# Performance work log

Hardware: AMD Instinct MI355X
Metric: run time of the kernel (lower is better)

## Reference

```python
import jax, jax.numpy as jnp
import numpy as np

EMBED_DIM = 2048
NUM_HEADS = 16
NUM_GROUPS = 4
HEAD_DIM = EMBED_DIM // NUM_HEADS  # 128
B, S = 2, 2048


def setup_inputs() -> dict:
    key = jax.random.key(0)
    ks = jax.random.split(key, 7)
    sc = 0.02
    return {
        "x": jax.random.normal(ks[0], (B, S, EMBED_DIM), dtype=jnp.float32),
        "Wq": jax.random.normal(ks[1], (EMBED_DIM, EMBED_DIM), dtype=jnp.float32) * sc,
        "bq": jnp.zeros((EMBED_DIM,), dtype=jnp.float32),
        "Wkv": jax.random.normal(ks[2], (EMBED_DIM, 2 * EMBED_DIM // NUM_GROUPS), dtype=jnp.float32) * sc,
        "bkv": jnp.zeros((2 * EMBED_DIM // NUM_GROUPS,), dtype=jnp.float32),
        "Wo": jax.random.normal(ks[3], (EMBED_DIM, EMBED_DIM), dtype=jnp.float32) * sc,
        "bo": jnp.zeros((EMBED_DIM,), dtype=jnp.float32),
    }


def reference(x, Wq, bq, Wkv, bkv, Wo, bo):
    b, s, e = x.shape
    group_size = NUM_HEADS // NUM_GROUPS
    # projections (torch Linear: x @ W + b with W stored [in, out] here)
    q = (x @ Wq + bq).reshape(b, s, NUM_HEADS, HEAD_DIM).transpose(0, 2, 1, 3)   # [B,H,S,D]
    kv = (x @ Wkv + bkv).reshape(b, s, NUM_GROUPS, 2 * HEAD_DIM).transpose(0, 2, 1, 3)  # [B,G,S,2D]
    k, v = kv[..., :HEAD_DIM], kv[..., HEAD_DIM:]                                # [B,G,S,D]
    # repeat each kv group for its heads (matches repeat_interleave on head dim)
    k = jnp.repeat(k, group_size, axis=1)                                        # [B,H,S,D]
    v = jnp.repeat(v, group_size, axis=1)                                        # [B,H,S,D]
    scores = jnp.einsum("bhqd,bhkd->bhqk", q, k) / (HEAD_DIM ** 0.5)             # [B,H,S,S]
    attn = jax.nn.softmax(scores, axis=-1)
    out = jnp.einsum("bhqk,bhkd->bhqd", attn, v)                                 # [B,H,S,D]
    out = out.transpose(0, 2, 1, 3).reshape(b, s, e)
    return out @ Wo + bo
```

## Files before the change

kernel.cpp:

```cpp
#include <hip/hip_runtime.h>

#define DEV __device__ __forceinline__

typedef unsigned short u16;
typedef unsigned int u32;
using bf16x8 = __attribute__((ext_vector_type(8))) __bf16;
using f32x4v = __attribute__((ext_vector_type(4))) float;

typedef __attribute__((address_space(1))) void gas_void;
typedef __attribute__((address_space(3))) void las_void;

DEV u16 f32_bf16(float f){
  u32 u = __float_as_uint(f);
  u += 0x7FFFu + ((u >> 16) & 1u);
  return (u16)(u >> 16);
}
DEV float bf16_f32(u16 h){ return __uint_as_float(((u32)h) << 16); }

DEV void gload16(const void* g, void* l){
  __builtin_amdgcn_global_load_lds((gas_void*)g, (las_void*)l, 16, 0, 0);
}

__global__ void cvt_f32_bf16_k(const float* __restrict__ in, u16* __restrict__ out, int n){
  int i = (blockIdx.x * 256 + threadIdx.x) * 8;
  if (i >= n) return;
  float4 a = *(const float4*)(in + i);
  float4 b = *(const float4*)(in + i + 4);
  uint4 r;
  r.x = (u32)f32_bf16(a.x) | ((u32)f32_bf16(a.y) << 16);
  r.y = (u32)f32_bf16(a.z) | ((u32)f32_bf16(a.w) << 16);
  r.z = (u32)f32_bf16(b.x) | ((u32)f32_bf16(b.y) << 16);
  r.w = (u32)f32_bf16(b.z) | ((u32)f32_bf16(b.w) << 16);
  *(uint4*)(out + i) = r;
}

template<typename T>
__global__ void transpose_cvt_k(const T* __restrict__ in, u16* __restrict__ out, int R, int C){
  in  += (size_t)blockIdx.z * R * C;
  out += (size_t)blockIdx.z * R * C;
  __shared__ float tile[64][65];
  int c0 = blockIdx.x * 64, r0 = blockIdx.y * 64;
  int t = threadIdx.x;
  int lr = t >> 4;
  int lc = (t & 15) * 4;
  #pragma unroll
  for (int p = 0; p < 4; p++){
    int row = p * 16 + lr;
    const T* src = in + (size_t)(r0 + row) * C + c0 + lc;
    float v0, v1, v2, v3;
    if constexpr (sizeof(T) == 4){
      float4 v = *(const float4*)src;
      v0 = v.x; v1 = v.y; v2 = v.z; v3 = v.w;
    } else {
      ushort4 v = *(const ushort4*)src;
      v0 = bf16_f32(v.x); v1 = bf16_f32(v.y); v2 = bf16_f32(v.z); v3 = bf16_f32(v.w);
    }
    tile[row][lc+0] = v0; tile[row][lc+1] = v1; tile[row][lc+2] = v2; tile[row][lc+3] = v3;
  }
  __syncthreads();
  #pragma unroll
  for (int p = 0; p < 4; p++){
    int ocol = p * 16 + lr;
    ushort4 w;
    w.x = f32_bf16(tile[lc+0][ocol]);
    w.y = f32_bf16(tile[lc+1][ocol]);
    w.z = f32_bf16(tile[lc+2][ocol]);
    w.w = f32_bf16(tile[lc+3][ocol]);
    *(ushort4*)(out + (size_t)(c0 + ocol) * R + r0 + lc) = w;
  }
}

__global__ __launch_bounds__(256, 2)
void gemm_bf16_k(const u16* __restrict__ A, const u16* __restrict__ BT,
                 const float* __restrict__ bias,
                 u16* __restrict__ outU0, u16* __restrict__ outU1,
                 float* __restrict__ outF,
                 int M, int N, int K, int mode)
{
  __shared__ __align__(16) u16 sA[2][128*32];
  __shared__ __align__(16) u16 sB[2][128*32];
  const int t = threadIdx.x;
  const int l = t & 63;
  const int wv = t >> 6;
  const int wm = wv >> 1, wn = wv & 1;
  const int rl = l & 15, gr = l >> 4;
  const size_t m0 = (size_t)blockIdx.x * 128, n0 = (size_t)blockIdx.y * 128;

  const u16* gA = A + m0 * K;
  const u16* gB = BT + n0 * K;

  f32x4v acc[4][4];
  #pragma unroll
  for (int i = 0; i < 4; i++)
    #pragma unroll
    for (int j = 0; j < 4; j++)
      acc[i][j] = (f32x4v)(0.0f);

  auto stage = [&](int buf, int kt){
    const size_t k0 = (size_t)kt * 32;
    #pragma unroll
    for (int i = 0; i < 2; i++){
      int c = i * 256 + t;
      int row = c >> 2, kc = c & 3;
      gload16(gA + (size_t)row * K + k0 + kc * 8, &sA[buf][c * 8]);
      gload16(gB + (size_t)row * K + k0 + kc * 8, &sB[buf][c * 8]);
    }
  };

  auto compute = [&](int buf){
    const u16* sa = sA[buf];
    const u16* sb = sB[buf];
    bf16x8 af[4], bfr[4];
    #pragma unroll
    for (int mr = 0; mr < 4; mr++)
      af[mr] = *(const bf16x8*)(sa + (wm*64 + mr*16 + rl)*32 + gr*8);
    #pragma unroll
    for (int nr = 0; nr < 4; nr++)
      bfr[nr] = *(const bf16x8*)(sb + (wn*64 + nr*16 + rl)*32 + gr*8);
    __builtin_amdgcn_s_setprio(1);
    #pragma unroll
    for (int mr = 0; mr < 4; mr++)
      #pragma unroll
      for (int nr = 0; nr < 4; nr++)
        acc[mr][nr] = __builtin_amdgcn_mfma_f32_16x16x32_bf16(af[mr], bfr[nr], acc[mr][nr], 0, 0, 0);
    __builtin_amdgcn_s_setprio(0);
  };

  stage(0, 0);
  asm volatile("s_waitcnt vmcnt(0)" ::: "memory");
  __syncthreads();
  const int NT = K / 32;
  for (int kt = 0; kt < NT; kt++){
    int cur = kt & 1;
    if (kt + 1 < NT) stage(cur ^ 1, kt + 1);
    compute(cur);
    asm volatile("s_waitcnt vmcnt(0)" ::: "memory");
    __syncthreads();
  }

  #pragma unroll
  for (int nr = 0; nr < 4; nr++){
    int col = (int)n0 + wn*64 + nr*16 + rl;
    float bv = bias[col];
    #pragma unroll
    for (int mr = 0; mr < 4; mr++){
      int rowb = (int)m0 + wm*64 + mr*16 + gr*4;
      #pragma unroll
      for (int r = 0; r < 4; r++){
        int row = rowb + r;
        float v = acc[mr][nr][r] + bv;
        if (mode == 2){
          outF[(size_t)row * N + col] = v;
        } else if (mode == 0){
          int b = row >> 11, s = row & 2047, h = col >> 7, d = col & 127;
          outU0[(((size_t)(b*16 + h)) * 2048 + s) * 128 + d] = f32_bf16(v);
        } else {
          int b = row >> 11, s = row & 2047, g = col >> 8, c = col & 255;
          u16* dst = (c < 128) ? outU0 : outU1;
          dst[(((size_t)(b*4 + g)) * 2048 + s) * 128 + (c & 127)] = f32_bf16(v);
        }
      }
    }
  }
}

__global__ __launch_bounds__(256, 2)
void attn_k(const u16* __restrict__ Q, const u16* __restrict__ Kb,
            const u16* __restrict__ VT, u16* __restrict__ O)
{
  __shared__ __align__(16) u16 sK[2][64*128];
  __shared__ __align__(16) u16 sV[2][128*64];
  __shared__ __align__(16) u16 Plds[4][16*72];
  const int t = threadIdx.x, l = t & 63, wv = t >> 6;
  const int rl = l & 15, gr = l >> 4;
  const int bh = blockIdx.y;
  const int b = bh >> 4, h = bh & 15, g = h >> 2;
  const int q0 = blockIdx.x * 64 + wv * 16;
  const u16* Qp = Q + ((size_t)(b*16 + h) * 2048 + q0) * 128;
  const u16* Kp = Kb + (size_t)(b*4 + g) * 2048 * 128;
  const u16* Vp = VT + (size_t)(b*4 + g) * 128 * 2048;

  bf16x8 qf[4];
  #pragma unroll
  for (int ds = 0; ds < 4; ds++)
    qf[ds] = *(const bf16x8*)(Qp + rl*128 + ds*32 + gr*8);

  f32x4v acc_o[8];
  #pragma unroll
  for (int i = 0; i < 8; i++) acc_o[i] = (f32x4v)(0.0f);
  float m_run = -3.0e38f, l_run = 0.0f;
  const float scale = 0.0883883476483184f;

  auto stageKV = [&](int buf, int kt){
    const int kv0 = kt * 64;
    const u16* Ksrc = Kp + (size_t)kv0 * 128;
    #pragma unroll
    for (int j = 0; j < 4; j++){
      int n16 = j * 256 + t;
      int row = n16 >> 4;
      int cl  = n16 & 15;
      int sc  = cl ^ (row & 7);
      gload16(Ksrc + row * 128 + sc * 8, &sK[buf][n16 * 8]);
    }
    const u16* Vsrc = Vp + kv0;
    #pragma unroll
    for (int j = 0; j < 4; j++){
      int n16 = j * 256 + t;
      int row = n16 >> 3;
      int cl  = n16 & 7;
      int sc  = cl ^ (row & 7);
      gload16(Vsrc + (size_t)row * 2048 + sc * 8, &sV[buf][n16 * 8]);
    }
  };

  stageKV(0, 0);
  asm volatile("s_waitcnt vmcnt(0)" ::: "memory");
  __syncthreads();

  for (int kt = 0; kt < 32; kt++){
    const int cur = kt & 1;
    if (kt + 1 < 32) stageKV(cur ^ 1, kt + 1);
    const u16* sk = sK[cur];
    const u16* sv = sV[cur];

    float pv[4][4];
    float tm = -3.0e38f;
    #pragma unroll
    for (int tt = 0; tt < 4; tt++){
      f32x4v st = (f32x4v)(0.0f);
      bf16x8 kf[4];
      #pragma unroll
      for (int ds = 0; ds < 4; ds++){
        int r = tt*16 + rl;
        int c = ds*4 + gr;
        kf[ds] = *(const bf16x8*)(sk + r*128 + ((c ^ (r & 7)) * 8));
      }
      __builtin_amdgcn_s_setprio(1);
      #pragma unroll
      for (int ds = 0; ds < 4; ds++)
        st = __builtin_amdgcn_mfma_f32_16x16x32_bf16(kf[ds], qf[ds], st, 0, 0, 0);
      __builtin_amdgcn_s_setprio(0);
      #pragma unroll
      for (int r = 0; r < 4; r++){
        float s = st[r] * scale;
        pv[tt][r] = s;
        tm = fmaxf(tm, s);
      }
    }
    tm = fmaxf(tm, __shfl_xor(tm, 16, 64));
    tm = fmaxf(tm, __shfl_xor(tm, 32, 64));
    float m_new = fmaxf(m_run, tm);
    float corr = __expf(m_run - m_new);
    float psum = 0.f;
    #pragma unroll
    for (int tt = 0; tt < 4; tt++)
      #pragma unroll
      for (int r = 0; r < 4; r++){
        float p = __expf(pv[tt][r] - m_new);
        pv[tt][r] = p;
        psum += p;
      }
    psum += __shfl_xor(psum, 16, 64);
    psum += __shfl_xor(psum, 32, 64);
    l_run = l_run * corr + psum;
    m_run = m_new;
    float cr0 = __shfl(corr, gr*4 + 0, 64);
    float cr1 = __shfl(corr, gr*4 + 1, 64);
    float cr2 = __shfl(corr, gr*4 + 2, 64);
    float cr3 = __shfl(corr, gr*4 + 3, 64);
    #pragma unroll
    for (int dc = 0; dc < 8; dc++){
      acc_o[dc][0] *= cr0; acc_o[dc][1] *= cr1; acc_o[dc][2] *= cr2; acc_o[dc][3] *= cr3;
    }
    #pragma unroll
    for (int tt = 0; tt < 4; tt++){
      ushort4 pk;
      pk.x = f32_bf16(pv[tt][0]); pk.y = f32_bf16(pv[tt][1]);
      pk.z = f32_bf16(pv[tt][2]); pk.w = f32_bf16(pv[tt][3]);
      *(ushort4*)&Plds[wv][rl*72 + tt*16 + gr*4] = pk;
    }
    asm volatile("s_waitcnt lgkmcnt(0)" ::: "memory");
    #pragma unroll
    for (int kc = 0; kc < 2; kc++){
      bf16x8 pa = *(const bf16x8*)&Plds[wv][rl*72 + kc*32 + gr*8];
      bf16x8 vf[8];
      #pragma unroll
      for (int dc = 0; dc < 8; dc++){
        int r = dc*16 + rl;
        int c = kc*4 + gr;
        vf[dc] = *(const bf16x8*)(sv + r*64 + ((c ^ (r & 7)) * 8));
      }
      __builtin_amdgcn_s_setprio(1);
      #pragma unroll
      for (int dc = 0; dc < 8; dc++)
        acc_o[dc] = __builtin_amdgcn_mfma_f32_16x16x32_bf16(pa, vf[dc], acc_o[dc], 0, 0, 0);
      __builtin_amdgcn_s_setprio(0);
    }
    asm volatile("s_waitcnt vmcnt(0)" ::: "memory");
    __syncthreads();
  }
  float linv = 1.0f / l_run;
  float lr0 = __shfl(linv, gr*4 + 0, 64);
  float lr1 = __shfl(linv, gr*4 + 1, 64);
  float lr2 = __shfl(linv, gr*4 + 2, 64);
  float lr3 = __shfl(linv, gr*4 + 3, 64);
  float lrr[4] = {lr0, lr1, lr2, lr3};
  #pragma unroll
  for (int dc = 0; dc < 8; dc++)
    #pragma unroll
    for (int r = 0; r < 4; r++){
      size_t idx = ((size_t)b * 2048 + q0 + gr*4 + r) * 2048 + h*128 + dc*16 + rl;
      O[idx] = f32_bf16(acc_o[dc][r] * lrr[r]);
    }
}

extern "C" void kernel_launch(void* const* d_in, const int* in_sizes, int n_in,
                              void* d_out, int out_size, void* d_ws, size_t ws_size,
                              hipStream_t stream)
{
  const float* x   = (const float*)d_in[0];
  const float* Wq  = (const float*)d_in[1];
  const float* bq  = (const float*)d_in[2];
  const float* Wkv = (const float*)d_in[3];
  const float* bkv = (const float*)d_in[4];
  const float* Wo  = (const float*)d_in[5];
  const float* bo  = (const float*)d_in[6];
  float* out = (float*)d_out;

  char* ws = (char*)d_ws;
  size_t off = 0;
  auto alloc = [&](size_t bytes){ void* p = ws + off; off = (off + bytes + 255) & ~(size_t)255; return p; };
  u16* xb   = (u16*)alloc(8388608ull * 2);
  u16* WqT  = (u16*)alloc(4194304ull * 2);
  u16* WkvT = (u16*)alloc(2097152ull * 2);
  u16* WoT  = (u16*)alloc(4194304ull * 2);
  u16* Qb   = (u16*)alloc(8388608ull * 2);
  u16* Kb   = (u16*)alloc(2097152ull * 2);
  u16* Vb   = (u16*)alloc(2097152ull * 2);
  u16* VTb  = (u16*)alloc(2097152ull * 2);
  u16* Ob   = (u16*)alloc(8388608ull * 2);

  cvt_f32_bf16_k<<<4096, 256, 0, stream>>>(x, xb, 8388608);
  transpose_cvt_k<float><<<dim3(32, 32, 1), 256, 0, stream>>>(Wq,  WqT,  2048, 2048);
  transpose_cvt_k<float><<<dim3(16, 32, 1), 256, 0, stream>>>(Wkv, WkvT, 2048, 1024);
  transpose_cvt_k<float><<<dim3(32, 32, 1), 256, 0, stream>>>(Wo,  WoT,  2048, 2048);

  gemm_bf16_k<<<dim3(32, 16), 256, 0, stream>>>(xb, WqT,  bq,  Qb, nullptr, nullptr, 4096, 2048, 2048, 0);
  gemm_bf16_k<<<dim3(32, 8),  256, 0, stream>>>(xb, WkvT, bkv, Kb, Vb,      nullptr, 4096, 1024, 2048, 1);

  transpose_cvt_k<u16><<<dim3(2, 32, 8), 256, 0, stream>>>(Vb, VTb, 2048, 128);

  attn_k<<<dim3(32, 32), 256, 0, stream>>>(Qb, Kb, VTb, Ob);

  gemm_bf16_k<<<dim3(32, 16), 256, 0, stream>>>(Ob, WoT, bo, nullptr, nullptr, out, 4096, 2048, 2048, 2);
}
```

Measured before the change: 391.0 us.

## Fuse QKV GEMM, enlarge GEMM tiles, and use exp2 with lazy rescale in attention

Concatenates Wq and Wkv so Q, K and V come from one GEMM launch, and replaces the 128x128 double-buffered GEMM with a 256x256-tile, 512-thread kernel. The new kernel uses a 4-deep LDS ring with a prefetch distance of two and swizzled LDS layout. In attention, the softmax scale and log2(e) are folded into Q at projection time so scores go straight to hardware exp2. The running-max rescale of the accumulator is skipped when the new max stays within a threshold of the old one. This cuts GEMM launch count, global traffic per FLOP and softmax ALU work, at the cost of much larger LDS per block, lower occupancy, and a tolerance-based skip of rescaling.

New measurement: 354.2 us. -9.4%, faster.

```diff
diff --git a/kernel.cpp b/kernel.cpp
--- a/kernel.cpp
+++ b/kernel.cpp
@@ -20,6 +20,14 @@
 DEV void gload16(const void* g, void* l){
   __builtin_amdgcn_global_load_lds((gas_void*)g, (las_void*)l, 16, 0, 0);
 }
+
+DEV float exp2_hw(float x){
+  float r;
+  asm("v_exp_f32 %0, %1" : "=v"(r) : "v"(x));
+  return r;
+}
+
+#define QSCL 0.12752333f
 
 __global__ void cvt_f32_bf16_k(const float* __restrict__ in, u16* __restrict__ out, int n){
   int i = (blockIdx.x * 256 + threadIdx.x) * 8;
@@ -70,94 +78,107 @@
   }
 }
 
-__global__ __launch_bounds__(256, 2)
-void gemm_bf16_k(const u16* __restrict__ A, const u16* __restrict__ BT,
-                 const float* __restrict__ bias,
-                 u16* __restrict__ outU0, u16* __restrict__ outU1,
-                 float* __restrict__ outF,
-                 int M, int N, int K, int mode)
+__global__ __launch_bounds__(512, 2)
+void gemm256_k(const u16* __restrict__ A, const u16* __restrict__ BT,
+               const float* __restrict__ bias0, const float* __restrict__ bias1,
+               u16* __restrict__ outQ, u16* __restrict__ outK, u16* __restrict__ outV,
+               float* __restrict__ outF, int K, int mode)
 {
-  __shared__ __align__(16) u16 sA[2][128*32];
-  __shared__ __align__(16) u16 sB[2][128*32];
+  __shared__ __align__(16) u16 sA[4][256*32];
+  __shared__ __align__(16) u16 sB[4][256*32];
   const int t = threadIdx.x;
-  const int l = t & 63;
-  const int wv = t >> 6;
-  const int wm = wv >> 1, wn = wv & 1;
+  const int l = t & 63, wv = t >> 6;
+  const int wm = wv >> 2, wn = wv & 3;
   const int rl = l & 15, gr = l >> 4;
-  const size_t m0 = (size_t)blockIdx.x * 128, n0 = (size_t)blockIdx.y * 128;
-
+  const size_t m0 = (size_t)blockIdx.x * 256, n0 = (size_t)blockIdx.y * 256;
   const u16* gA = A + m0 * K;
   const u16* gB = BT + n0 * K;
 
-  f32x4v acc[4][4];
-  #pragma unroll
-  for (int i = 0; i < 4; i++)
+  const u16* gAs[2]; const u16* gBs[2]; int ldso[2];
+  #pragma unroll
+  for (int j = 0; j < 2; j++){
+    int c = t + j * 512;
+    int row = c >> 2, cl = c & 3;
+    int clp = cl ^ ((row >> 1) & 3);
+    gAs[j] = gA + (size_t)row * K + clp * 8;
+    gBs[j] = gB + (size_t)row * K + clp * 8;
+    ldso[j] = c * 8;
+  }
+  auto stage = [&](int kt){
+    int buf = kt & 3;
+    int k0 = kt * 32;
+    #pragma unroll
+    for (int j = 0; j < 2; j++){
+      gload16(gAs[j] + k0, &sA[buf][ldso[j]]);
+      gload16(gBs[j] + k0, &sB[buf][ldso[j]]);
+    }
+  };
+
+  const int swz8 = (gr ^ ((rl >> 1) & 3)) * 8;
+  int offA[8], offB[4];
+  #pragma unroll
+  for (int mr = 0; mr < 8; mr++) offA[mr] = (wm*128 + mr*16 + rl) * 32 + swz8;
+  #pragma unroll
+  for (int nr = 0; nr < 4; nr++) offB[nr] = (wn*64 + nr*16 + rl) * 32 + swz8;
+
+  f32x4v acc[8][4];
+  #pragma unroll
+  for (int i = 0; i < 8; i++)
     #pragma unroll
     for (int j = 0; j < 4; j++)
       acc[i][j] = (f32x4v)(0.0f);
 
-  auto stage = [&](int buf, int kt){
-    const size_t k0 = (size_t)kt * 32;
-    #pragma unroll
-    for (int i = 0; i < 2; i++){
-      int c = i * 256 + t;
-      int row = c >> 2, kc = c & 3;
-      gload16(gA + (size_t)row * K + k0 + kc * 8, &sA[buf][c * 8]);
-      gload16(gB + (size_t)row * K + k0 + kc * 8, &sB[buf][c * 8]);
-    }
-  };
-
-  auto compute = [&](int buf){
-    const u16* sa = sA[buf];
-    const u16* sb = sB[buf];
-    bf16x8 af[4], bfr[4];
-    #pragma unroll
-    for (int mr = 0; mr < 4; mr++)
-      af[mr] = *(const bf16x8*)(sa + (wm*64 + mr*16 + rl)*32 + gr*8);
-    #pragma unroll
-    for (int nr = 0; nr < 4; nr++)
-      bfr[nr] = *(const bf16x8*)(sb + (wn*64 + nr*16 + rl)*32 + gr*8);
+  const int NT = K / 32;
+  stage(0); stage(1);
+  asm volatile("s_waitcnt vmcnt(4)" ::: "memory");
+  __builtin_amdgcn_s_barrier();
+
+  for (int kt = 0; kt < NT; kt++){
+    const u16* sa = sA[kt & 3];
+    const u16* sb = sB[kt & 3];
+    bf16x8 af[8], bfr[4];
+    #pragma unroll
+    for (int mr = 0; mr < 8; mr++) af[mr] = *(const bf16x8*)(sa + offA[mr]);
+    #pragma unroll
+    for (int nr = 0; nr < 4; nr++) bfr[nr] = *(const bf16x8*)(sb + offB[nr]);
+    if (kt + 2 < NT){
+      stage(kt + 2);
+      asm volatile("s_waitcnt vmcnt(4)" ::: "memory");
+    } else {
+      asm volatile("s_waitcnt vmcnt(0)" ::: "memory");
+    }
+    __builtin_amdgcn_s_barrier();
     __builtin_amdgcn_s_setprio(1);
     #pragma unroll
-    for (int mr = 0; mr < 4; mr++)
+    for (int mr = 0; mr < 8; mr++)
       #pragma unroll
       for (int nr = 0; nr < 4; nr++)
         acc[mr][nr] = __builtin_amdgcn_mfma_f32_16x16x32_bf16(af[mr], bfr[nr], acc[mr][nr], 0, 0, 0);
     __builtin_amdgcn_s_setprio(0);
-  };
-
-  stage(0, 0);
-  asm volatile("s_waitcnt vmcnt(0)" ::: "memory");
-  __syncthreads();
-  const int NT = K / 32;
-  for (int kt = 0; kt < NT; kt++){
-    int cur = kt & 1;
-    if (kt + 1 < NT) stage(cur ^ 1, kt + 1);
-    compute(cur);
-    asm volatile("s_waitcnt vmcnt(0)" ::: "memory");
-    __syncthreads();
   }
 
   #pragma unroll
   for (int nr = 0; nr < 4; nr++){
     int col = (int)n0 + wn*64 + nr*16 + rl;
-    float bv = bias[col];
-    #pragma unroll
-    for (int mr = 0; mr < 4; mr++){
-      int rowb = (int)m0 + wm*64 + mr*16 + gr*4;
+    float bv = (mode == 2 || col < 2048) ? bias0[col < 2048 ? col : 0] : 0.0f;
+    if (mode != 2 && col >= 2048) bv = bias1[col - 2048];
+    #pragma unroll
+    for (int mr = 0; mr < 8; mr++){
+      int rowb = (int)m0 + wm*128 + mr*16 + gr*4;
       #pragma unroll
       for (int r = 0; r < 4; r++){
         int row = rowb + r;
         float v = acc[mr][nr][r] + bv;
         if (mode == 2){
-          outF[(size_t)row * N + col] = v;
-        } else if (mode == 0){
+          outF[(size_t)row * 2048 + col] = v;
+        } else if (col < 2048){
           int b = row >> 11, s = row & 2047, h = col >> 7, d = col & 127;
-          outU0[(((size_t)(b*16 + h)) * 2048 + s) * 128 + d] = f32_bf16(v);
+          outQ[(((size_t)(b*16 + h)) * 2048 + s) * 128 + d] = f32_bf16(v * QSCL);
         } else {
-          int b = row >> 11, s = row & 2047, g = col >> 8, c = col & 255;
-          u16* dst = (c < 128) ? outU0 : outU1;
-          dst[(((size_t)(b*4 + g)) * 2048 + s) * 128 + (c & 127)] = f32_bf16(v);
+          int b = row >> 11, s = row & 2047;
+          int c2 = col - 2048, g = c2 >> 8, cc = c2 & 255;
+          u16* dst = (cc < 128) ? outK : outV;
+          dst[(((size_t)(b*4 + g)) * 2048 + s) * 128 + (cc & 127)] = f32_bf16(v);
         }
       }
     }
@@ -189,7 +210,6 @@
   #pragma unroll
   for (int i = 0; i < 8; i++) acc_o[i] = (f32x4v)(0.0f);
   float m_run = -3.0e38f, l_run = 0.0f;
-  const float scale = 0.0883883476483184f;
 
   auto stageKV = [&](int buf, int kt){
     const int kv0 = kt * 64;
@@ -197,18 +217,16 @@
     #pragma unroll
     for (int j = 0; j < 4; j++){
       int n16 = j * 256 + t;
-      int row = n16 >> 4;
-      int cl  = n16 & 15;
-      int sc  = cl ^ (row & 7);
+      int row = n16 >> 4, cl = n16 & 15;
+      int sc = cl ^ (row & 7);
       gload16(Ksrc + row * 128 + sc * 8, &sK[buf][n16 * 8]);
     }
     const u16* Vsrc = Vp + kv0;
     #pragma unroll
     for (int j = 0; j < 4; j++){
       int n16 = j * 256 + t;
-      int row = n16 >> 3;
-      int cl  = n16 & 7;
-      int sc  = cl ^ (row & 7);
+      int row = n16 >> 3, cl = n16 & 7;
+      int sc = cl ^ (row & 7);
       gload16(Vsrc + (size_t)row * 2048 + sc * 8, &sV[buf][n16 * 8]);
     }
   };
@@ -242,36 +260,39 @@
       __builtin_amdgcn_s_setprio(0);
       #pragma unroll
       for (int r = 0; r < 4; r++){
-        float s = st[r] * scale;
-        pv[tt][r] = s;
-        tm = fmaxf(tm, s);
+        pv[tt][r] = st[r];
+        tm = fmaxf(tm, st[r]);
       }
     }
     tm = fmaxf(tm, __shfl_xor(tm, 16, 64));
     tm = fmaxf(tm, __shfl_xor(tm, 32, 64));
-    float m_new = fmaxf(m_run, tm);
-    float corr = __expf(m_run - m_new);
+    if (!__all(tm <= m_run + 11.0f)){
+      float m_new = fmaxf(m_run, tm);
+      float corr = exp2_hw(m_run - m_new);
+      l_run *= corr;
+      float cr0 = __shfl(corr, gr*4 + 0, 64);
+      float cr1 = __shfl(corr, gr*4 + 1, 64);
+      float cr2 = __shfl(corr, gr*4 + 2, 64);
+      float cr3 = __shfl(corr, gr*4 + 3, 64);
+      #pragma unroll
+      for (int dc = 0; dc < 8; dc++){
+        acc_o[dc][0] *= cr0; acc_o[dc][1] *= cr1; acc_o[dc][2] *= cr2; acc_o[dc][3] *= cr3;
+      }
+      m_run = m_new;
+    }
     float psum = 0.f;
     #pragma unroll
     for (int tt = 0; tt < 4; tt++)
       #pragma unroll
       for (int r = 0; r < 4; r++){
-        float p = __expf(pv[tt][r] - m_new);
+        float p = exp2_hw(pv[tt][r] - m_run);
         pv[tt][r] = p;
         psum += p;
       }
     psum += __shfl_xor(psum, 16, 64);
     psum += __shfl_xor(psum, 32, 64);
-    l_run = l_run * corr + psum;
-    m_run = m_new;
-    float cr0 = __shfl(corr, gr*4 + 0, 64);
-    float cr1 = __shfl(corr, gr*4 + 1, 64);
-    float cr2 = __shfl(corr, gr*4 + 2, 64);
-    float cr3 = __shfl(corr, gr*4 + 3, 64);
-    #pragma unroll
-    for (int dc = 0; dc < 8; dc++){
-      acc_o[dc][0] *= cr0; acc_o[dc][1] *= cr1; acc_o[dc][2] *= cr2; acc_o[dc][3] *= cr3;
-    }
+    l_run += psum;
+
     #pragma unroll
     for (int tt = 0; tt < 4; tt++){
       ushort4 pk;
@@ -330,27 +351,25 @@
   char* ws = (char*)d_ws;
   size_t off = 0;
   auto alloc = [&](size_t bytes){ void* p = ws + off; off = (off + bytes + 255) & ~(size_t)255; return p; };
-  u16* xb   = (u16*)alloc(8388608ull * 2);
-  u16* WqT  = (u16*)alloc(4194304ull * 2);
-  u16* WkvT = (u16*)alloc(2097152ull * 2);
-  u16* WoT  = (u16*)alloc(4194304ull * 2);
-  u16* Qb   = (u16*)alloc(8388608ull * 2);
-  u16* Kb   = (u16*)alloc(2097152ull * 2);
-  u16* Vb   = (u16*)alloc(2097152ull * 2);
-  u16* VTb  = (u16*)alloc(2097152ull * 2);
-  u16* Ob   = (u16*)alloc(8388608ull * 2);
+  u16* xb     = (u16*)alloc(8388608ull * 2);
+  u16* WqkvT  = (u16*)alloc(6291456ull * 2);
+  u16* WoT    = (u16*)alloc(4194304ull * 2);
+  u16* Qb     = (u16*)alloc(8388608ull * 2);
+  u16* Kb     = (u16*)alloc(2097152ull * 2);
+  u16* Vb     = (u16*)alloc(2097152ull * 2);
+  u16* VTb    = (u16*)alloc(2097152ull * 2);
+  u16* Ob     = (u16*)alloc(8388608ull * 2);
 
   cvt_f32_bf16_k<<<4096, 256, 0, stream>>>(x, xb, 8388608);
-  transpose_cvt_k<float><<<dim3(32, 32, 1), 256, 0, stream>>>(Wq,  WqT,  2048, 2048);
-  transpose_cvt_k<float><<<dim3(16, 32, 1), 256, 0, stream>>>(Wkv, WkvT, 2048, 1024);
-  transpose_cvt_k<float><<<dim3(32, 32, 1), 256, 0, stream>>>(Wo,  WoT,  2048, 2048);
-
-  gemm_bf16_k<<<dim3(32, 16), 256, 0, stream>>>(xb, WqT,  bq,  Qb, nullptr, nullptr, 4096, 2048, 2048, 0);
-  gemm_bf16_k<<<dim3(32, 8),  256, 0, stream>>>(xb, WkvT, bkv, Kb, Vb,      nullptr, 4096, 1024, 2048, 1);
+  transpose_cvt_k<float><<<dim3(32, 32, 1), 256, 0, stream>>>(Wq,  WqkvT, 2048, 2048);
+  transpose_cvt_k<float><<<dim3(16, 32, 1), 256, 0, stream>>>(Wkv, WqkvT + 2048ull*2048ull, 2048, 1024);
+  transpose_cvt_k<float><<<dim3(32, 32, 1), 256, 0, stream>>>(Wo,  WoT, 2048, 2048);
+
+  gemm256_k<<<dim3(16, 12), 512, 0, stream>>>(xb, WqkvT, bq, bkv, Qb, Kb, Vb, nullptr, 2048, 0);
 
   transpose_cvt_k<u16><<<dim3(2, 32, 8), 256, 0, stream>>>(Vb, VTb, 2048, 128);
 
   attn_k<<<dim3(32, 32), 256, 0, stream>>>(Qb, Kb, VTb, Ob);
 
-  gemm_bf16_k<<<dim3(32, 16), 256, 0, stream>>>(Ob, WoT, bo, nullptr, nullptr, out, 4096, 2048, 2048, 2);
-}
+  gemm256_k<<<dim3(16, 8), 512, 0, stream>>>(Ob, WoT, bo, nullptr, nullptr, nullptr, nullptr, out, 2048, 2);
+}
```
